# Kernel optimization log

Measured on AMD Instinct MI355X. Metric: run time of the kernel, lower is better.

## Reference

```python
import jax, jax.numpy as jnp
import numpy as np

# LIF dynamics constants (match init_kwargs)
STEPS = 20          # T // dt
DT = 1.0
TAU_M = 20.0
TAU_S = 5.0
THRESH = 1.0
SUR_ALPHA = 10.0    # surrogate-gradient sharpness (stand-in for custom spikeprop bwd)

@jax.custom_vjp
def spike_fn(v):
    # Heaviside threshold; nondifferentiable, custom vjp supplies surrogate grad
    return (v >= THRESH).astype(v.dtype)

def _spike_fwd(v):
    return spike_fn(v), v

def _spike_bwd(v, g):
    # fast-sigmoid (SuperSpike) surrogate derivative centered at threshold
    sur = 1.0 / (1.0 + SUR_ALPHA * jnp.abs(v - THRESH)) ** 2
    return (g * sur,)

spike_fn.defvjp(_spike_fwd, _spike_bwd)


def setup_inputs() -> dict:
    key = jax.random.key(0)
    k1, k2 = jax.random.split(key)
    # Bernoulli(0.1) rate-coded input spike train: [steps, batch, input_dim]
    x = (jax.random.uniform(k1, (STEPS, 512, 2048)) < 0.1).astype(jnp.float32)
    # nn.init.normal_(weight, mean=mu, std=mu) with mu=0.1; W: [output_dim, input_dim]
    W = 0.1 + 0.1 * jax.random.normal(k2, (2048, 2048), dtype=jnp.float32)
    return {"x": x, "W": W}


def reference(x, W):
    # x: [steps, batch, input_dim] spikes; W: [out, in]
    a_m = 1.0 - DT / TAU_M   # membrane decay
    a_s = 1.0 - DT / TAU_S   # synaptic decay
    B = x.shape[1]
    O = W.shape[0]

    def step(carry, x_t):
        V, I = carry                       # [B, O] each
        V_new = a_m * V + (DT / TAU_M) * I # leaky integration of synaptic current
        s = spike_fn(V_new)                # threshold crossing -> spikes
        V_new = V_new * (1.0 - s)          # reset-to-zero on spike
        I_new = a_s * I + x_t @ W.T        # synaptic current driven by input spikes
        return (V_new, I_new), s

    init = (jnp.zeros((B, O), x.dtype), jnp.zeros((B, O), x.dtype))
    _, spikes = jax.lax.scan(step, init, x)
    return spikes  # [steps, batch, output_dim]
```

## Files before the change

kernel.cpp:

```cpp
#include <hip/hip_runtime.h>
#include <stdint.h>


#define STEPS  20
#define BATCH  512
#define DIM    2048

#define XQ_OFF   0ULL
#define WQ_OFF   20971520ULL
#define C_OFF    37748736ULL

#define GLOBAL_AS __attribute__((address_space(1)))
#define LDS_AS    __attribute__((address_space(3)))

typedef int v4i  __attribute__((ext_vector_type(4)));
typedef int v16i __attribute__((ext_vector_type(16)));


__global__ __launch_bounds__(256)
void prep_x_kernel(const float* __restrict__ x, char* __restrict__ wsb)
{
    const int bid = blockIdx.x;
    const int kc = bid & 31, mt = bid >> 5;
    const int tid = threadIdx.x;
    char* outb = wsb + (size_t)bid * 8192;
#pragma unroll
    for (int it = 0; it < 8; ++it) {
        const int idx = it * 256 + tid;
        const int mm = idx >> 4;
        const int kk4 = (idx & 15) << 2;
        const float4 v = *reinterpret_cast<const float4*>(
            x + (size_t)(mt * 128 + mm) * DIM + kc * 64 + kk4);
        uchar4 o;
        o.x = (v.x != 0.0f); o.y = (v.y != 0.0f);
        o.z = (v.z != 0.0f); o.w = (v.w != 0.0f);
        *reinterpret_cast<uchar4*>(
            outb + (((kk4 >> 4) * 128 + mm) << 4) + (kk4 & 15)) = o;
    }
}

__global__ __launch_bounds__(256)
void prep_w_kernel(const float* __restrict__ W, char* __restrict__ wsb)
{
    const int bid = blockIdx.x;
    const int kc = bid & 31, nt = bid >> 5;
    const int tid = threadIdx.x;
    char* wqb = wsb + WQ_OFF;
#pragma unroll
    for (int it = 0; it < 8; ++it) {
        const int idx = it * 256 + tid;
        const int nn = idx >> 4;
        const int kk4 = (idx & 15) << 2;
        const float4 v = *reinterpret_cast<const float4*>(
            W + (size_t)(nt * 128 + nn) * DIM + kc * 64 + kk4);
        int dg[4][4];
        const float* vp = &v.x;
#pragma unroll
        for (int c = 0; c < 4; ++c) {
            long long q = __double2ll_rn((double)vp[c] * 2147483648.0);
#pragma unroll
            for (int j = 0; j < 3; ++j) {
                int d = (int)(q & 255);
                if (d >= 128) d -= 256;
                dg[c][j] = d;
                q = (q - d) >> 8;
            }
            dg[c][3] = (int)q;
        }
        const size_t sub = (size_t)(((kk4 >> 4) * 128 + nn) << 4) + (kk4 & 15);
#pragma unroll
        for (int j = 0; j < 4; ++j) {
            uchar4 o;
            o.x = (unsigned char)(dg[0][j] & 255);
            o.y = (unsigned char)(dg[1][j] & 255);
            o.z = (unsigned char)(dg[2][j] & 255);
            o.w = (unsigned char)(dg[3][j] & 255);
            *reinterpret_cast<uchar4*>(
                wqb + ((size_t)((j * 16 + nt) * 32 + kc)) * 8192 + sub) = o;
        }
    }
}

__global__ __launch_bounds__(256, 4)
void gemm_i8_kernel(const char* __restrict__ wsb_c, short* __restrict__ cp,
                    int nt0, int ntc_cnt, int no)
{
    __shared__ __align__(16) char lds[2][16384];

    const int bid = blockIdx.x;
    const int mt = bid % 80;
    const int rest = bid / 80;
    const int ntc = rest % ntc_cnt;
    const int limb = rest / ntc_cnt;

    const int tid = threadIdx.x;
    const int lane = tid & 63, w = tid >> 6;
    const int kh = lane >> 5, ln = lane & 31;
    const int wy = w & 1, wx = w >> 1;

    const char* abase = wsb_c + XQ_OFF + ((size_t)mt * 32) * 8192;
    const char* bbase = wsb_c + WQ_OFF
        + ((size_t)((limb * 16 + nt0 + ntc) * 32)) * 8192;

    const int aoff = ((kh * 128) + wy * 64 + ln) << 4;
    const int boff = ((kh * 128) + wx * 64 + ln) << 4;
    const int stg = (w * 2) * 1024 + (lane << 4);

    v16i acc00, acc01, acc10, acc11;
#pragma unroll
    for (int r = 0; r < 16; ++r) {
        acc00[r] = 0; acc01[r] = 0; acc10[r] = 0; acc11[r] = 0;
    }

    LDS_AS char* l0 = (LDS_AS char*)(&lds[0][0]);
    LDS_AS char* l1 = (LDS_AS char*)(&lds[1][0]);

#pragma unroll
    for (int i = 0; i < 2; ++i) {
        __builtin_amdgcn_global_load_lds(
            (const GLOBAL_AS void*)(abase + stg + i * 1024),
            (LDS_AS void*)(l0 + (w * 2 + i) * 1024), 16, 0, 0);
        __builtin_amdgcn_global_load_lds(
            (const GLOBAL_AS void*)(bbase + stg + i * 1024),
            (LDS_AS void*)(l0 + 8192 + (w * 2 + i) * 1024), 16, 0, 0);
    }

    for (int kc = 0; kc < 32; ++kc) {
        __syncthreads();
        const int cur = kc & 1;
        if (kc + 1 < 32) {
            LDS_AS char* ldst = (kc & 1) ? l0 : l1;
            const size_t src = (size_t)(kc + 1) * 8192 + stg;
#pragma unroll
            for (int i = 0; i < 2; ++i) {
                __builtin_amdgcn_global_load_lds(
                    (const GLOBAL_AS void*)(abase + src + i * 1024),
                    (LDS_AS void*)(ldst + (w * 2 + i) * 1024), 16, 0, 0);
                __builtin_amdgcn_global_load_lds(
                    (const GLOBAL_AS void*)(bbase + src + i * 1024),
                    (LDS_AS void*)(ldst + 8192 + (w * 2 + i) * 1024), 16, 0, 0);
            }
        }
        const char* A = &lds[cur][0];
        const char* B = &lds[cur][8192];
#pragma unroll
        for (int s = 0; s < 2; ++s) {
            const v4i a0 = *reinterpret_cast<const v4i*>(A + aoff + s * 4096);
            const v4i a1 = *reinterpret_cast<const v4i*>(A + aoff + 512 + s * 4096);
            const v4i b0 = *reinterpret_cast<const v4i*>(B + boff + s * 4096);
            const v4i b1 = *reinterpret_cast<const v4i*>(B + boff + 512 + s * 4096);
            acc00 = __builtin_amdgcn_mfma_i32_32x32x32_i8(a0, b0, acc00, 0, 0, 0);
            acc01 = __builtin_amdgcn_mfma_i32_32x32x32_i8(a0, b1, acc01, 0, 0, 0);
            acc10 = __builtin_amdgcn_mfma_i32_32x32x32_i8(a1, b0, acc10, 0, 0, 0);
            acc11 = __builtin_amdgcn_mfma_i32_32x32x32_i8(a1, b1, acc11, 0, 0, 0);
        }
    }

    short* cpl = cp + (size_t)limb * 10240 * no;
    const int m_base = mt * 128 + wy * 64;
    const int o_base = ntc * 128 + wx * 64 + ln;
#pragma unroll
    for (int r = 0; r < 16; ++r) {
        const int row = (r & 3) + ((r >> 2) << 3) + (kh << 2);
        const size_t m0 = (size_t)(m_base + row) * no;
        const size_t m1 = (size_t)(m_base + 32 + row) * no;
        cpl[m0 + o_base]      = (short)acc00[r];
        cpl[m0 + o_base + 32] = (short)acc01[r];
        cpl[m1 + o_base]      = (short)acc10[r];
        cpl[m1 + o_base + 32] = (short)acc11[r];
    }
}

__global__ __launch_bounds__(256)
void lif_kernel(const short* __restrict__ cp, float* __restrict__ out,
                int o0, int no, int shift)
{
    const int g = blockIdx.x * 256 + threadIdx.x;
    const int b = g >> shift;
    const int oq = g & ((1 << shift) - 1);
    const int o_local = oq << 2;
    const size_t plane = (size_t)10240 * no;

    const double A_M = 1.0 - 1.0 / 20.0;
    const double DTM = 1.0 / 20.0;
    const double A_S = 1.0 - 1.0 / 5.0;
    double V[4], I[4];
#pragma unroll
    for (int u = 0; u < 4; ++u) { V[u] = 0.0; I[u] = 0.0; }

#pragma unroll
    for (int t = 0; t < STEPS; ++t) {
        const size_t ix = (size_t)(t * BATCH + b) * no + o_local;
        const short4 c0 = *reinterpret_cast<const short4*>(cp + ix);
        const short4 c1 = *reinterpret_cast<const short4*>(cp + plane + ix);
        const short4 c2 = *reinterpret_cast<const short4*>(cp + 2 * plane + ix);
        const short4 c3 = *reinterpret_cast<const short4*>(cp + 3 * plane + ix);
        const short* p0 = &c0.x; const short* p1 = &c1.x;
        const short* p2 = &c2.x; const short* p3 = &c3.x;
        float4 s;
        float* sp = &s.x;
#pragma unroll
        for (int u = 0; u < 4; ++u) {
            const long long tot = (long long)p0[u]
                + ((long long)p1[u] << 8)
                + ((long long)p2[u] << 16)
                + ((long long)p3[u] << 24);
            const double val = (double)tot * 4.6566128730773926e-10;
            V[u] = A_M * V[u] + DTM * I[u];
            float sv = 0.0f;
            if (V[u] >= 1.0) { sv = 1.0f; V[u] = 0.0; }
            sp[u] = sv;
            I[u] = A_S * I[u] + val;
        }
        *reinterpret_cast<float4*>(
            out + (size_t)(t * BATCH + b) * DIM + o0 + o_local) = s;
    }
}


#define B_TILE 2
#define O_TILE 256
#define NT     512
#define KT     32
#define NSLAB  (DIM / KT)
#define ROWB   1024

__global__ __launch_bounds__(256)
void transpose_kernel(const float* __restrict__ W, float* __restrict__ WT)
{
    __shared__ float tile[64][65];
    const int tid = threadIdx.x;
    const int c4 = (tid & 15) * 4;
    const int rr = tid >> 4;
    const int k0 = blockIdx.x * 64, o0 = blockIdx.y * 64;
#pragma unroll
    for (int i = 0; i < 64; i += 16) {
        const float4 v = *reinterpret_cast<const float4*>(
            W + (size_t)(o0 + rr + i) * DIM + k0 + c4);
        tile[c4 + 0][rr + i] = v.x;
        tile[c4 + 1][rr + i] = v.y;
        tile[c4 + 2][rr + i] = v.z;
        tile[c4 + 3][rr + i] = v.w;
    }
    __syncthreads();
#pragma unroll
    for (int i = 0; i < 64; i += 16) {
        float4 v;
        v.x = tile[rr + i][c4 + 0];
        v.y = tile[rr + i][c4 + 1];
        v.z = tile[rr + i][c4 + 2];
        v.w = tile[rr + i][c4 + 3];
        *reinterpret_cast<float4*>(
            WT + (size_t)(k0 + rr + i) * DIM + o0 + c4) = v;
    }
}

__global__ __launch_bounds__(NT, 6)
void snn_lif_kernel(const float* __restrict__ x,
                    const float* __restrict__ WT,
                    float* __restrict__ out)
{
    __shared__ __align__(16) float wlds[(KT * ROWB) / 4];

    const int tid  = threadIdx.x;
    const int lane = tid & 63;
    const int w    = tid >> 6;
    const int bl   = w & 1;
    const int tq   = w >> 1;
    const int o_blk = blockIdx.x & 7;
    const int b_blk = blockIdx.x >> 3;
    const int b  = b_blk * B_TILE + bl;
    const int o0 = o_blk * O_TILE;

    double acc[5][4];
#pragma unroll
    for (int tt = 0; tt < 5; ++tt)
#pragma unroll
        for (int u = 0; u < 4; ++u) acc[tt][u] = 0.0;

    const int kl = lane & 31;
    float xr[5];
#pragma unroll
    for (int m = 0; m < 5; ++m)
        xr[m] = x[((size_t)(tq * 5 + m) * BATCH + b) * DIM + kl];

    const char*   gb   = (const char*)wlds + (lane << 4);
    LDS_AS char*  ldsb = (LDS_AS char*)wlds;
    const float*  wsrc = WT + o0 + (lane << 2);

    for (int kt = 0; kt < NSLAB; ++kt) {
        const int k0 = kt * KT;
        __syncthreads();
#pragma unroll
        for (int it = 0; it < 4; ++it) {
            const int r = w + it * 8;
            __builtin_amdgcn_global_load_lds(
                (const GLOBAL_AS void*)(wsrc + (size_t)(k0 + r) * DIM),
                (LDS_AS void*)(ldsb + r * ROWB), 16, 0, 0);
        }
        unsigned mk[5];
#pragma unroll
        for (int m = 0; m < 5; ++m)
            mk[m] = (unsigned)__ballot(xr[m] != 0.0f);
        __syncthreads();
        if (kt + 1 < NSLAB) {
            const int k1 = k0 + KT;
#pragma unroll
            for (int m = 0; m < 5; ++m)
                xr[m] = x[((size_t)(tq * 5 + m) * BATCH + b) * DIM + k1 + kl];
        }
#pragma unroll
        for (int m = 0; m < 5; ++m) {
            unsigned msk = mk[m];
            while (msk & (msk - 1)) {
                const int r0 = __builtin_ctz(msk); msk &= msk - 1;
                const int r1 = __builtin_ctz(msk); msk &= msk - 1;
                const float4 va = *reinterpret_cast<const float4*>(gb + (r0 << 10));
                const float4 vb = *reinterpret_cast<const float4*>(gb + (r1 << 10));
                acc[m][0] += (double)va.x; acc[m][1] += (double)va.y;
                acc[m][2] += (double)va.z; acc[m][3] += (double)va.w;
                acc[m][0] += (double)vb.x; acc[m][1] += (double)vb.y;
                acc[m][2] += (double)vb.z; acc[m][3] += (double)vb.w;
            }
            if (msk) {
                const int r = __builtin_ctz(msk);
                const float4 wv = *reinterpret_cast<const float4*>(gb + (r << 10));
                acc[m][0] += (double)wv.x; acc[m][1] += (double)wv.y;
                acc[m][2] += (double)wv.z; acc[m][3] += (double)wv.w;
            }
        }
    }

    const double A_M = 1.0 - 1.0 / 20.0;
    const double DTM = 1.0 / 20.0;
    const double A_S = 1.0 - 1.0 / 5.0;

    __syncthreads();
    double2* hand = reinterpret_cast<double2*>(wlds);
    const int hbase = bl * 256 + (lane << 2);
    const size_t obase = (size_t)o0 + (lane << 2);

    for (int seg = 0; seg < 4; ++seg) {
        if (tq == seg) {
            double V[4], I[4];
            if (seg == 0) {
#pragma unroll
                for (int u = 0; u < 4; ++u) { V[u] = 0.0; I[u] = 0.0; }
            } else {
#pragma unroll
                for (int u = 0; u < 4; ++u) {
                    const double2 h = hand[hbase + u];
                    V[u] = h.x; I[u] = h.y;
                }
            }
#pragma unroll
            for (int tt = 0; tt < 5; ++tt) {
                const int t = seg * 5 + tt;
                float4 s;
                float* sp = &s.x;
#pragma unroll
                for (int u = 0; u < 4; ++u) {
                    V[u] = A_M * V[u] + DTM * I[u];
                    float sv = 0.0f;
                    if (V[u] >= 1.0) { sv = 1.0f; V[u] = 0.0; }
                    sp[u] = sv;
                    I[u] = A_S * I[u] + acc[tt][u];
                }
                *reinterpret_cast<float4*>(
                    out + ((size_t)t * BATCH + b) * DIM + obase) = s;
            }
            if (seg < 3) {
#pragma unroll
                for (int u = 0; u < 4; ++u)
                    hand[hbase + u] = make_double2(V[u], I[u]);
            }
        }
        __syncthreads();
    }
}


extern "C" void kernel_launch(void* const* d_in, const int* in_sizes, int n_in,
                              void* d_out, int out_size, void* d_ws, size_t ws_size,
                              hipStream_t stream) {
    const float* x = (const float*)d_in[0];
    const float* W = (const float*)d_in[1];
    float* out = (float*)d_out;
    char* wsb = (char*)d_ws;

    int no = 0, shift = 0;
    if      (ws_size >= C_OFF + 81920ULL * 1024) { no = 1024; shift = 8; }
    else if (ws_size >= C_OFF + 81920ULL * 512)  { no = 512;  shift = 7; }
    else if (ws_size >= C_OFF + 81920ULL * 256)  { no = 256;  shift = 6; }
    else if (ws_size >= C_OFF + 81920ULL * 128)  { no = 128;  shift = 5; }

    if (no) {
        prep_x_kernel<<<2560, 256, 0, stream>>>(x, wsb);
        prep_w_kernel<<<512, 256, 0, stream>>>(W, wsb);
        short* cp = (short*)(wsb + C_OFF);
        const int ntc_cnt = no / 128;
        for (int nt0 = 0; nt0 < 16; nt0 += ntc_cnt) {
            gemm_i8_kernel<<<4 * ntc_cnt * 80, 256, 0, stream>>>(
                (const char*)wsb, cp, nt0, ntc_cnt, no);
            lif_kernel<<<no / 2, 256, 0, stream>>>(
                (const short*)cp, out, nt0 * 128, no, shift);
        }
    } else {
        float* WT = (float*)d_ws;
        dim3 tb(256);
        dim3 tg(DIM / 64, DIM / 64);
        transpose_kernel<<<tg, tb, 0, stream>>>(W, WT);
        const int grid = (BATCH / B_TILE) * (DIM / O_TILE);
        snn_lif_kernel<<<grid, NT, 0, stream>>>(x, WT, out);
    }
}
```

Before: 339.0 us.

## Process two weight limbs per GEMM block to reuse A tiles

Each GEMM block now computes two of the four weight limbs at once, sharing the loaded x (A) tile across both and keeping eight accumulators. This halves the grid and the redundant A-tile traffic, at the cost of a larger LDS footprint and more registers, so occupancy is lowered to 2 blocks per CU. A 2048-wide output chunk option is also added when the workspace is large enough, which cuts the number of GEMM/LIF launch pairs.

```diff
diff --git a/kernel.cpp b/kernel.cpp
--- a/kernel.cpp
+++ b/kernel.cpp
@@ -81,17 +81,17 @@
     }
 }
 
-__global__ __launch_bounds__(256, 4)
+__global__ __launch_bounds__(256, 2)
 void gemm_i8_kernel(const char* __restrict__ wsb_c, short* __restrict__ cp,
                     int nt0, int ntc_cnt, int no)
 {
-    __shared__ __align__(16) char lds[2][16384];
+    __shared__ __align__(16) char lds[2][24576];
 
     const int bid = blockIdx.x;
     const int mt = bid % 80;
     const int rest = bid / 80;
     const int ntc = rest % ntc_cnt;
-    const int limb = rest / ntc_cnt;
+    const int pair = rest / ntc_cnt;
 
     const int tid = threadIdx.x;
     const int lane = tid & 63, w = tid >> 6;
@@ -99,17 +99,21 @@
     const int wy = w & 1, wx = w >> 1;
 
     const char* abase = wsb_c + XQ_OFF + ((size_t)mt * 32) * 8192;
-    const char* bbase = wsb_c + WQ_OFF
-        + ((size_t)((limb * 16 + nt0 + ntc) * 32)) * 8192;
+    const char* bbase0 = wsb_c + WQ_OFF
+        + ((size_t)(((pair * 2 + 0) * 16 + nt0 + ntc) * 32)) * 8192;
+    const char* bbase1 = wsb_c + WQ_OFF
+        + ((size_t)(((pair * 2 + 1) * 16 + nt0 + ntc) * 32)) * 8192;
 
     const int aoff = ((kh * 128) + wy * 64 + ln) << 4;
     const int boff = ((kh * 128) + wx * 64 + ln) << 4;
     const int stg = (w * 2) * 1024 + (lane << 4);
 
-    v16i acc00, acc01, acc10, acc11;
+    v16i acc0_00, acc0_01, acc0_10, acc0_11;
+    v16i acc1_00, acc1_01, acc1_10, acc1_11;
 #pragma unroll
     for (int r = 0; r < 16; ++r) {
-        acc00[r] = 0; acc01[r] = 0; acc10[r] = 0; acc11[r] = 0;
+        acc0_00[r] = 0; acc0_01[r] = 0; acc0_10[r] = 0; acc0_11[r] = 0;
+        acc1_00[r] = 0; acc1_01[r] = 0; acc1_10[r] = 0; acc1_11[r] = 0;
     }
 
     LDS_AS char* l0 = (LDS_AS char*)(&lds[0][0]);
@@ -121,8 +125,11 @@
             (const GLOBAL_AS void*)(abase + stg + i * 1024),
             (LDS_AS void*)(l0 + (w * 2 + i) * 1024), 16, 0, 0);
         __builtin_amdgcn_global_load_lds(
-            (const GLOBAL_AS void*)(bbase + stg + i * 1024),
+            (const GLOBAL_AS void*)(bbase0 + stg + i * 1024),
             (LDS_AS void*)(l0 + 8192 + (w * 2 + i) * 1024), 16, 0, 0);
+        __builtin_amdgcn_global_load_lds(
+            (const GLOBAL_AS void*)(bbase1 + stg + i * 1024),
+            (LDS_AS void*)(l0 + 16384 + (w * 2 + i) * 1024), 16, 0, 0);
     }
 
     for (int kc = 0; kc < 32; ++kc) {
@@ -137,26 +144,38 @@
                     (const GLOBAL_AS void*)(abase + src + i * 1024),
                     (LDS_AS void*)(ldst + (w * 2 + i) * 1024), 16, 0, 0);
                 __builtin_amdgcn_global_load_lds(
-                    (const GLOBAL_AS void*)(bbase + src + i * 1024),
+                    (const GLOBAL_AS void*)(bbase0 + src + i * 1024),
                     (LDS_AS void*)(ldst + 8192 + (w * 2 + i) * 1024), 16, 0, 0);
-            }
-        }
-        const char* A = &lds[cur][0];
-        const char* B = &lds[cur][8192];
+                __builtin_amdgcn_global_load_lds(
+                    (const GLOBAL_AS void*)(bbase1 + src + i * 1024),
+                    (LDS_AS void*)(ldst + 16384 + (w * 2 + i) * 1024), 16, 0, 0);
+            }
+        }
+        const char* A  = &lds[cur][0];
+        const char* B0 = &lds[cur][8192];
+        const char* B1 = &lds[cur][16384];
 #pragma unroll
         for (int s = 0; s < 2; ++s) {
-            const v4i a0 = *reinterpret_cast<const v4i*>(A + aoff + s * 4096);
-            const v4i a1 = *reinterpret_cast<const v4i*>(A + aoff + 512 + s * 4096);
-            const v4i b0 = *reinterpret_cast<const v4i*>(B + boff + s * 4096);
-            const v4i b1 = *reinterpret_cast<const v4i*>(B + boff + 512 + s * 4096);
-            acc00 = __builtin_amdgcn_mfma_i32_32x32x32_i8(a0, b0, acc00, 0, 0, 0);
-            acc01 = __builtin_amdgcn_mfma_i32_32x32x32_i8(a0, b1, acc01, 0, 0, 0);
-            acc10 = __builtin_amdgcn_mfma_i32_32x32x32_i8(a1, b0, acc10, 0, 0, 0);
-            acc11 = __builtin_amdgcn_mfma_i32_32x32x32_i8(a1, b1, acc11, 0, 0, 0);
-        }
-    }
-
-    short* cpl = cp + (size_t)limb * 10240 * no;
+            const v4i a0  = *reinterpret_cast<const v4i*>(A  + aoff + s * 4096);
+            const v4i a1  = *reinterpret_cast<const v4i*>(A  + aoff + 512 + s * 4096);
+            const v4i b00 = *reinterpret_cast<const v4i*>(B0 + boff + s * 4096);
+            const v4i b01 = *reinterpret_cast<const v4i*>(B0 + boff + 512 + s * 4096);
+            const v4i b10 = *reinterpret_cast<const v4i*>(B1 + boff + s * 4096);
+            const v4i b11 = *reinterpret_cast<const v4i*>(B1 + boff + 512 + s * 4096);
+            acc0_00 = __builtin_amdgcn_mfma_i32_32x32x32_i8(a0, b00, acc0_00, 0, 0, 0);
+            acc0_01 = __builtin_amdgcn_mfma_i32_32x32x32_i8(a0, b01, acc0_01, 0, 0, 0);
+            acc0_10 = __builtin_amdgcn_mfma_i32_32x32x32_i8(a1, b00, acc0_10, 0, 0, 0);
+            acc0_11 = __builtin_amdgcn_mfma_i32_32x32x32_i8(a1, b01, acc0_11, 0, 0, 0);
+            acc1_00 = __builtin_amdgcn_mfma_i32_32x32x32_i8(a0, b10, acc1_00, 0, 0, 0);
+            acc1_01 = __builtin_amdgcn_mfma_i32_32x32x32_i8(a0, b11, acc1_01, 0, 0, 0);
+            acc1_10 = __builtin_amdgcn_mfma_i32_32x32x32_i8(a1, b10, acc1_10, 0, 0, 0);
+            acc1_11 = __builtin_amdgcn_mfma_i32_32x32x32_i8(a1, b11, acc1_11, 0, 0, 0);
+        }
+    }
+
+    const size_t plane = (size_t)10240 * no;
+    short* cpl0 = cp + (size_t)(pair * 2 + 0) * plane;
+    short* cpl1 = cp + (size_t)(pair * 2 + 1) * plane;
     const int m_base = mt * 128 + wy * 64;
     const int o_base = ntc * 128 + wx * 64 + ln;
 #pragma unroll
@@ -164,10 +183,14 @@
         const int row = (r & 3) + ((r >> 2) << 3) + (kh << 2);
         const size_t m0 = (size_t)(m_base + row) * no;
         const size_t m1 = (size_t)(m_base + 32 + row) * no;
-        cpl[m0 + o_base]      = (short)acc00[r];
-        cpl[m0 + o_base + 32] = (short)acc01[r];
-        cpl[m1 + o_base]      = (short)acc10[r];
-        cpl[m1 + o_base + 32] = (short)acc11[r];
+        cpl0[m0 + o_base]      = (short)acc0_00[r];
+        cpl0[m0 + o_base + 32] = (short)acc0_01[r];
+        cpl0[m1 + o_base]      = (short)acc0_10[r];
+        cpl0[m1 + o_base + 32] = (short)acc0_11[r];
+        cpl1[m0 + o_base]      = (short)acc1_00[r];
+        cpl1[m0 + o_base + 32] = (short)acc1_01[r];
+        cpl1[m1 + o_base]      = (short)acc1_10[r];
+        cpl1[m1 + o_base + 32] = (short)acc1_11[r];
     }
 }
 
@@ -389,7 +412,8 @@
     char* wsb = (char*)d_ws;
 
     int no = 0, shift = 0;
-    if      (ws_size >= C_OFF + 81920ULL * 1024) { no = 1024; shift = 8; }
+    if      (ws_size >= C_OFF + 81920ULL * 2048) { no = 2048; shift = 9; }
+    else if (ws_size >= C_OFF + 81920ULL * 1024) { no = 1024; shift = 8; }
     else if (ws_size >= C_OFF + 81920ULL * 512)  { no = 512;  shift = 7; }
     else if (ws_size >= C_OFF + 81920ULL * 256)  { no = 256;  shift = 6; }
     else if (ws_size >= C_OFF + 81920ULL * 128)  { no = 128;  shift = 5; }
@@ -400,7 +424,7 @@
         short* cp = (short*)(wsb + C_OFF);
         const int ntc_cnt = no / 128;
         for (int nt0 = 0; nt0 < 16; nt0 += ntc_cnt) {
-            gemm_i8_kernel<<<4 * ntc_cnt * 80, 256, 0, stream>>>(
+            gemm_i8_kernel<<<2 * ntc_cnt * 80, 256, 0, stream>>>(
                 (const char*)wsb, cp, nt0, ntc_cnt, no);
             lif_kernel<<<no / 2, 256, 0, stream>>>(
                 (const short*)cp, out, nt0 * 128, no, shift);
```

Result: no change. 342.5 us (+1.0%).
